# Kernel optimization log

Measured on AMD Instinct MI355X. Metric: run time of the kernel, lower is better.

Reference implementation:

```python
import jax, jax.numpy as jnp
import numpy as np

N = 200000
C = 384
G = 383            # number of unique target ids (0..G-1 all present w.h.p.)
M = G + 1          # object_num = len(unique) + 1; must equal C for the original broadcast
EPS = 1e-5


def setup_inputs() -> dict:
    key = jax.random.key(0)
    k1, k2 = jax.random.split(key)
    pred_id = jax.random.normal(k1, (N, C), dtype=jnp.float32)
    target_id = jax.random.randint(k2, (N,), 0, G)
    return {"pred_id": pred_id, "target_id": target_id}


def reference(pred_id, target_id):
    seg = target_id  # ids are 0..G-1 and all present -> sorted unique == arange(G)
    dt = pred_id.dtype
    ones = jnp.ones((N,), dtype=dt)
    n_rows = jax.ops.segment_sum(ones, seg, num_segments=G)                 # [G] group sizes
    row_sum = jax.ops.segment_sum(pred_id.sum(axis=1), seg, num_segments=G)  # [G]
    cnt = n_rows * C                                                        # elements per group
    mean = row_sum / cnt                                                    # scalar mean per group
    centered = pred_id - mean[seg][:, None]
    ss = jax.ops.segment_sum((centered * centered).sum(axis=1), seg, num_segments=G)
    # torch .std() is unbiased over all n_i*C elements; 0 if group has a single row
    std = jnp.where(n_rows > 1, jnp.sqrt(ss / jnp.maximum(cnt - 1.0, 1.0)), 0.0)

    # pad the extra (always-zero) object slot -> object_proto/object_std have M rows
    proto = jnp.concatenate([mean, jnp.zeros((1,), dt)])   # [M]; each row of object_proto is constant
    stdv = jnp.concatenate([std, jnp.zeros((1,), dt)])     # [M]

    diff = proto[None, :] - proto[:, None]                 # [M,M] V_dist[x,a,:] is constant over C
    norm = jnp.abs(diff) * jnp.sqrt(jnp.asarray(C, dt))    # ||V_dist||_2 over C channels
    d = jax.lax.stop_gradient(diff / (norm + EPS))         # detached unit direction, [M,M]

    # object_std_i[x,a,b] = |std[a] * d[x,a]|; object_std_j[x,a,b] = |std[b] * d[x,a]|
    si = jnp.abs(stdv[None, :, None] * d[:, :, None])      # [M,M,M]
    sj = jnp.abs(stdv[None, None, :] * d[:, :, None])      # [M,M,M]
    s = si + sj
    V = s / (norm[None, :, :] + s + EPS)                   # V_dist_norm broadcast as [1,M,M]
    mask = jnp.triu(jnp.ones((M, M), dtype=bool), k=1)     # triu(diagonal=1) on last two dims
    V = jnp.where(mask[None, :, :], V, jnp.zeros((), dt))
    return V.mean()
```

## Files before the change

### kernel.cpp

```cpp
#include <hip/hip_runtime.h>
#include <math.h>

#define NROWS 200000
#define C 384
#define G 383
#define M 384
#define EPS 1e-5f
#define SQRTC 19.595917942265423f

#define NBLK1 1024
#define THR1 512
#define NWAVES ((NBLK1 * THR1) / 64)
#define NBLK4 576

#define WS_PART  0
#define WS_S2    (WS_PART + NBLK1 * 1152)
#define WS_PROTO (WS_S2 + 8 * 1152)
#define WS_STD   (WS_PROTO + 384)
#define WS_P3    (WS_STD + 384)

__global__ __launch_bounds__(THR1) void stats_kernel(const float4* __restrict__ pred4,
                                                     const int* __restrict__ tgt,
                                                     float* __restrict__ ws,
                                                     int n_rows) {
    __shared__ float lc[384], ls[384], lq[384];
    const int tid = threadIdx.x;
    for (int i = tid; i < 384; i += THR1) { lc[i] = 0.f; ls[i] = 0.f; lq[i] = 0.f; }
    __syncthreads();

    const int lane = tid & 63;
    const int wv   = (blockIdx.x * THR1 + tid) >> 6;

    for (int row = wv; row < n_rows; row += NWAVES) {
        const float4* rp = pred4 + (size_t)row * 96;
        const int seg = tgt[row];
        float4 v0 = rp[lane];
        float s = (v0.x + v0.y) + (v0.z + v0.w);
        float q = fmaf(v0.x, v0.x, fmaf(v0.y, v0.y, fmaf(v0.z, v0.z, v0.w * v0.w)));
        if (lane < 32) {
            float4 v1 = rp[64 + lane];
            s += (v1.x + v1.y) + (v1.z + v1.w);
            q += fmaf(v1.x, v1.x, fmaf(v1.y, v1.y, fmaf(v1.z, v1.z, v1.w * v1.w)));
        }
#pragma unroll
        for (int off = 32; off > 0; off >>= 1) {
            s += __shfl_down(s, off);
            q += __shfl_down(q, off);
        }
        if (lane == 0) {
            atomicAdd(&lc[seg], 1.0f);
            atomicAdd(&ls[seg], s);
            atomicAdd(&lq[seg], q);
        }
    }
    __syncthreads();

    float* dst = ws + (size_t)blockIdx.x * 1152;
    for (int i = tid; i < 384; i += THR1) {
        dst[i]       = lc[i];
        dst[384 + i] = ls[i];
        dst[768 + i] = lq[i];
    }
}

__global__ void reduce_kernel(float* __restrict__ ws) {
    const int t   = blockIdx.x * blockDim.x + threadIdx.x;
    const int j   = t % 1152;
    const int sub = t / 1152;
    float acc = 0.f;
#pragma unroll 8
    for (int b = sub; b < NBLK1; b += 8)
        acc += ws[WS_PART + (size_t)b * 1152 + j];
    ws[WS_S2 + sub * 1152 + j] = acc;
}

__global__ void finalize_kernel(float* __restrict__ ws) {
    const int g = threadIdx.x;
    float cnt_r = 0.f, sum = 0.f, ss = 0.f;
#pragma unroll
    for (int sub = 0; sub < 8; ++sub) {
        const float* s2 = ws + WS_S2 + sub * 1152;
        cnt_r += s2[g];
        sum   += s2[384 + g];
        ss    += s2[768 + g];
    }
    float mean = 0.f, sd = 0.f;
    if (g < G && cnt_r > 0.5f) {
        float cnt = cnt_r * (float)C;
        mean = sum / cnt;
        if (cnt_r > 1.5f) {
            float cs    = ss - cnt * mean * mean;
            float denom = fmaxf(cnt - 1.0f, 1.0f);
            sd = sqrtf(fmaxf(cs / denom, 0.f));
        }
    }
    ws[WS_PROTO + g] = mean;
    ws[WS_STD + g]   = sd;
}

__global__ void triple_sum_kernel(const float* __restrict__ ws,
                                  float* __restrict__ part3) {
    __shared__ float sp[M];
    __shared__ float sst[M];
    __shared__ float wsum[4];
    const int tid = threadIdx.x;

    for (int i = tid; i < M; i += blockDim.x) {
        sp[i]  = ws[WS_PROTO + i];
        sst[i] = ws[WS_STD + i];
    }
    __syncthreads();

    const int idx = blockIdx.x * blockDim.x + tid;
    float partial = 0.f;
    {
        const int x = idx / M;
        const int a = idx - x * M;
        const float pa = sp[a];
        const float u  = fabsf(pa - sp[x]);
        const float t  = u / (u * SQRTC + EPS);
        if (t > 0.f) {
            const float sa = sst[a];
#pragma unroll 4
            for (int b = a + 1; b < M; ++b) {
                float nab = fabsf(sp[b] - pa) * SQRTC;
                float s   = t * (sa + sst[b]);
                partial += s * __builtin_amdgcn_rcpf(nab + s + EPS);
            }
        }
    }

#pragma unroll
    for (int off = 32; off > 0; off >>= 1)
        partial += __shfl_down(partial, off);
    if ((tid & 63) == 0) wsum[tid >> 6] = partial;
    __syncthreads();
    if (tid == 0)
        part3[blockIdx.x] = wsum[0] + wsum[1] + wsum[2] + wsum[3];
}

__global__ void write_out_kernel(const float* __restrict__ part3,
                                 float* __restrict__ out) {
    __shared__ float wsum[9];
    const int tid = threadIdx.x;
    float v = part3[tid];
#pragma unroll
    for (int off = 32; off > 0; off >>= 1)
        v += __shfl_down(v, off);
    if ((tid & 63) == 0) wsum[tid >> 6] = v;
    __syncthreads();
    if (tid == 0) {
        float acc = 0.f;
#pragma unroll
        for (int w = 0; w < 9; ++w) acc += wsum[w];
        out[0] = acc / ((float)M * (float)M * (float)M);
    }
}

extern "C" void kernel_launch(void* const* d_in, const int* in_sizes, int n_in,
                              void* d_out, int out_size, void* d_ws, size_t ws_size,
                              hipStream_t stream) {
    const float4* pred4 = (const float4*)d_in[0];
    const int*    tgt   = (const int*)d_in[1];
    float* ws  = (float*)d_ws;
    float* out = (float*)d_out;
    const int n_rows = in_sizes[1];

    stats_kernel<<<NBLK1, THR1, 0, stream>>>(pred4, tgt, ws, n_rows);
    reduce_kernel<<<36, 256, 0, stream>>>(ws);
    finalize_kernel<<<1, 384, 0, stream>>>(ws);
    triple_sum_kernel<<<NBLK4, 256, 0, stream>>>(ws, ws + WS_P3);
    write_out_kernel<<<1, 576, 0, stream>>>(ws + WS_P3, out);
}
```

Baseline: 436.0 us.

## Process row pairs per wave and fuse partial reduction into finalize via transposed layout

The stats kernel now has each wave handle two rows at once. It loads three full float4 vectors per lane so that no lanes sit idle, which they did before when only half the wave loaded the second chunk. Per-block partials are written transposed (stat-major, block-minor), so a new 384-block finalize kernel can reduce each group's 1024 partials with coalesced float4 loads. This removes the separate reduce kernel launch. The row count is now hardcoded to NROWS/2, which assumes an even, fixed input size.

After: 438.1 us. About the same (+0.5%).

```diff
diff --git a/kernel.cpp b/kernel.cpp
--- a/kernel.cpp
+++ b/kernel.cpp
@@ -11,91 +11,111 @@
 #define NBLK1 1024
 #define THR1 512
 #define NWAVES ((NBLK1 * THR1) / 64)
+#define NPAIRS (NROWS / 2)
 #define NBLK4 576
 
 #define WS_PART  0
-#define WS_S2    (WS_PART + NBLK1 * 1152)
-#define WS_PROTO (WS_S2 + 8 * 1152)
+#define WS_PROTO (1152 * NBLK1)
 #define WS_STD   (WS_PROTO + 384)
 #define WS_P3    (WS_STD + 384)
 
 __global__ __launch_bounds__(THR1) void stats_kernel(const float4* __restrict__ pred4,
                                                      const int* __restrict__ tgt,
                                                      float* __restrict__ ws,
-                                                     int n_rows) {
-    __shared__ float lc[384], ls[384], lq[384];
+                                                     int n_pairs) {
+    __shared__ float l[1152];
     const int tid = threadIdx.x;
-    for (int i = tid; i < 384; i += THR1) { lc[i] = 0.f; ls[i] = 0.f; lq[i] = 0.f; }
+    for (int i = tid; i < 1152; i += THR1) l[i] = 0.f;
     __syncthreads();
 
     const int lane = tid & 63;
     const int wv   = (blockIdx.x * THR1 + tid) >> 6;
 
-    for (int row = wv; row < n_rows; row += NWAVES) {
-        const float4* rp = pred4 + (size_t)row * 96;
-        const int seg = tgt[row];
+    for (int p = wv; p < n_pairs; p += NWAVES) {
+        const float4* rp = pred4 + (size_t)p * 192;
         float4 v0 = rp[lane];
-        float s = (v0.x + v0.y) + (v0.z + v0.w);
-        float q = fmaf(v0.x, v0.x, fmaf(v0.y, v0.y, fmaf(v0.z, v0.z, v0.w * v0.w)));
-        if (lane < 32) {
-            float4 v1 = rp[64 + lane];
-            s += (v1.x + v1.y) + (v1.z + v1.w);
-            q += fmaf(v1.x, v1.x, fmaf(v1.y, v1.y, fmaf(v1.z, v1.z, v1.w * v1.w)));
-        }
+        float4 v1 = rp[64 + lane];
+        float4 v2 = rp[128 + lane];
+
+        float s1 = (v1.x + v1.y) + (v1.z + v1.w);
+        float q1 = fmaf(v1.x, v1.x, fmaf(v1.y, v1.y, fmaf(v1.z, v1.z, v1.w * v1.w)));
+        bool lowhalf = (lane < 32);
+
+        float sA = (v0.x + v0.y) + (v0.z + v0.w) + (lowhalf ? s1 : 0.f);
+        float qA = fmaf(v0.x, v0.x, fmaf(v0.y, v0.y, fmaf(v0.z, v0.z, v0.w * v0.w)))
+                 + (lowhalf ? q1 : 0.f);
+        float sB = (v2.x + v2.y) + (v2.z + v2.w) + (lowhalf ? 0.f : s1);
+        float qB = fmaf(v2.x, v2.x, fmaf(v2.y, v2.y, fmaf(v2.z, v2.z, v2.w * v2.w)))
+                 + (lowhalf ? 0.f : q1);
+
 #pragma unroll
         for (int off = 32; off > 0; off >>= 1) {
-            s += __shfl_down(s, off);
-            q += __shfl_down(q, off);
+            sA += __shfl_down(sA, off);
+            qA += __shfl_down(qA, off);
+            sB += __shfl_down(sB, off);
+            qB += __shfl_down(qB, off);
         }
         if (lane == 0) {
-            atomicAdd(&lc[seg], 1.0f);
-            atomicAdd(&ls[seg], s);
-            atomicAdd(&lq[seg], q);
+            int segA = tgt[2 * p];
+            int segB = tgt[2 * p + 1];
+            atomicAdd(&l[segA], 1.0f);
+            atomicAdd(&l[384 + segA], sA);
+            atomicAdd(&l[768 + segA], qA);
+            atomicAdd(&l[segB], 1.0f);
+            atomicAdd(&l[384 + segB], sB);
+            atomicAdd(&l[768 + segB], qB);
         }
     }
     __syncthreads();
 
-    float* dst = ws + (size_t)blockIdx.x * 1152;
-    for (int i = tid; i < 384; i += THR1) {
-        dst[i]       = lc[i];
-        dst[384 + i] = ls[i];
-        dst[768 + i] = lq[i];
-    }
+    const int blk = blockIdx.x;
+    for (int i = tid; i < 1152; i += THR1)
+        ws[WS_PART + (size_t)i * NBLK1 + blk] = l[i];
 }
 
-__global__ void reduce_kernel(float* __restrict__ ws) {
-    const int t   = blockIdx.x * blockDim.x + threadIdx.x;
-    const int j   = t % 1152;
-    const int sub = t / 1152;
-    float acc = 0.f;
-#pragma unroll 8
-    for (int b = sub; b < NBLK1; b += 8)
-        acc += ws[WS_PART + (size_t)b * 1152 + j];
-    ws[WS_S2 + sub * 1152 + j] = acc;
-}
+__global__ __launch_bounds__(256) void finalize_kernel(float* __restrict__ ws) {
+    __shared__ float wred[4][3];
+    const int g   = blockIdx.x;
+    const int tid = threadIdx.x;
 
-__global__ void finalize_kernel(float* __restrict__ ws) {
-    const int g = threadIdx.x;
-    float cnt_r = 0.f, sum = 0.f, ss = 0.f;
+    const float4* cnt_row = (const float4*)(ws + WS_PART + (size_t)g * NBLK1);
+    const float4* sum_row = (const float4*)(ws + WS_PART + (size_t)(384 + g) * NBLK1);
+    const float4* ss_row  = (const float4*)(ws + WS_PART + (size_t)(768 + g) * NBLK1);
+
+    float4 c4 = cnt_row[tid], s4 = sum_row[tid], q4 = ss_row[tid];
+    float c = (c4.x + c4.y) + (c4.z + c4.w);
+    float s = (s4.x + s4.y) + (s4.z + s4.w);
+    float q = (q4.x + q4.y) + (q4.z + q4.w);
+
 #pragma unroll
-    for (int sub = 0; sub < 8; ++sub) {
-        const float* s2 = ws + WS_S2 + sub * 1152;
-        cnt_r += s2[g];
-        sum   += s2[384 + g];
-        ss    += s2[768 + g];
+    for (int off = 32; off > 0; off >>= 1) {
+        c += __shfl_down(c, off);
+        s += __shfl_down(s, off);
+        q += __shfl_down(q, off);
     }
-    float mean = 0.f, sd = 0.f;
-    if (g < G && cnt_r > 0.5f) {
-        float cnt = cnt_r * (float)C;
-        mean = sum / cnt;
-        if (cnt_r > 1.5f) {
-            float cs    = ss - cnt * mean * mean;
-            float denom = fmaxf(cnt - 1.0f, 1.0f);
-            sd = sqrtf(fmaxf(cs / denom, 0.f));
+    if ((tid & 63) == 0) {
+        wred[tid >> 6][0] = c;
+        wred[tid >> 6][1] = s;
+        wred[tid >> 6][2] = q;
+    }
+    __syncthreads();
+    if (tid == 0) {
+        float cnt_r = wred[0][0] + wred[1][0] + wred[2][0] + wred[3][0];
+        float sum   = wred[0][1] + wred[1][1] + wred[2][1] + wred[3][1];
+        float ss    = wred[0][2] + wred[1][2] + wred[2][2] + wred[3][2];
+        float mean = 0.f, sd = 0.f;
+        if (g < G && cnt_r > 0.5f) {
+            float cnt = cnt_r * (float)C;
+            mean = sum / cnt;
+            if (cnt_r > 1.5f) {
+                float cs    = ss - cnt * mean * mean;
+                float denom = fmaxf(cnt - 1.0f, 1.0f);
+                sd = sqrtf(fmaxf(cs / denom, 0.f));
+            }
         }
+        ws[WS_PROTO + g] = mean;
+        ws[WS_STD + g]   = sd;
     }
-    ws[WS_PROTO + g] = mean;
-    ws[WS_STD + g]   = sd;
 }
 
 __global__ void triple_sum_kernel(const float* __restrict__ ws,
@@ -164,11 +184,9 @@
     const int*    tgt   = (const int*)d_in[1];
     float* ws  = (float*)d_ws;
     float* out = (float*)d_out;
-    const int n_rows = in_sizes[1];
 
-    stats_kernel<<<NBLK1, THR1, 0, stream>>>(pred4, tgt, ws, n_rows);
-    reduce_kernel<<<36, 256, 0, stream>>>(ws);
-    finalize_kernel<<<1, 384, 0, stream>>>(ws);
+    stats_kernel<<<NBLK1, THR1, 0, stream>>>(pred4, tgt, ws, NPAIRS);
+    finalize_kernel<<<384, 256, 0, stream>>>(ws);
     triple_sum_kernel<<<NBLK4, 256, 0, stream>>>(ws, ws + WS_P3);
     write_out_kernel<<<1, 576, 0, stream>>>(ws + WS_P3, out);
 }
```
